# Optimization experiments

Measured on AMD Instinct MI355X. Metric: run time of the kernel, lower is better.

Reference implementation:

```python
import jax, jax.numpy as jnp
import numpy as np

N_SPARSE = 2  # keep N of every M weights (2:4 structured sparsity)
M_SPARSE = 4


def compute_mask(w, n, m):
    # w: [out, in]; zero the (m - n) smallest-|w| entries in each group of m
    out_f, in_f = w.shape
    k = m - n
    wr = jnp.abs(w).reshape(out_f, in_f // m, m)
    # indices of the k smallest |w| per group (torch.topk largest=False)
    _, idx = jax.lax.top_k(-wr, k)                      # [out, in/m, k]
    pruned = jax.nn.one_hot(idx, m, dtype=w.dtype).sum(axis=-2)  # [out, in/m, m]
    mask = 1.0 - pruned
    return mask.reshape(out_f, in_f)


def setup_inputs() -> dict:
    key = jax.random.key(0)
    k1, k2, k3 = jax.random.split(key, 3)
    B, S, Din, Dout = 64, 197, 768, 3072
    x = jax.random.normal(k1, (B, S, Din), dtype=jnp.float32)
    weight = jax.random.normal(k2, (Dout, Din), dtype=jnp.float32)
    bias = jax.random.normal(k3, (Dout,), dtype=jnp.float32)
    return {"x": x, "weight": weight, "bias": bias}


def reference(x, weight, bias):
    # mask is a precomputed buffer in torch (not differentiated)
    mask = compute_mask(jax.lax.stop_gradient(weight), N_SPARSE, M_SPARSE)
    w = weight * mask
    # F.linear: x @ w.T + b
    return jnp.einsum('bsi,oi->bso', x, w) + bias
```

## Files before the change

kernel.cpp:

```cpp
#include <hip/hip_runtime.h>
#include <hip/hip_bf16.h>

#define M_DIM 12608
#define K_DIM 768
#define N_DIM 3072
#define M_PAD 12672
#define BM 128
#define BN 128
#define BK 32

typedef __attribute__((ext_vector_type(8))) short bf16x8;
typedef __attribute__((ext_vector_type(4))) float f32x4;

__device__ __forceinline__ void gload_lds16(const void* g, void* l) {
  __builtin_amdgcn_global_load_lds(
      (const __attribute__((address_space(1))) unsigned int*)g,
      (__attribute__((address_space(3))) unsigned int*)l,
      16, 0, 0);
}

__global__ void cvt_x(const float* __restrict__ x, __hip_bfloat16* __restrict__ xb) {
  size_t i = ((size_t)blockIdx.x * blockDim.x + threadIdx.x) * 8;
  if (i >= (size_t)M_PAD * K_DIM) return;
  union { __hip_bfloat16 h[8]; uint4 u; } o;
  if (i < (size_t)M_DIM * K_DIM) {
    float4 a = *(const float4*)(x + i);
    float4 b = *(const float4*)(x + i + 4);
    o.h[0] = __float2bfloat16(a.x); o.h[1] = __float2bfloat16(a.y);
    o.h[2] = __float2bfloat16(a.z); o.h[3] = __float2bfloat16(a.w);
    o.h[4] = __float2bfloat16(b.x); o.h[5] = __float2bfloat16(b.y);
    o.h[6] = __float2bfloat16(b.z); o.h[7] = __float2bfloat16(b.w);
  } else {
    o.u = make_uint4(0, 0, 0, 0);
  }
  *(uint4*)(xb + i) = o.u;
}

__global__ void cvt_w(const float* __restrict__ w, __hip_bfloat16* __restrict__ wb) {
  size_t g = (size_t)blockIdx.x * blockDim.x + threadIdx.x;
  if (g >= (size_t)N_DIM * (K_DIM / 4)) return;
  float4 v = *(const float4*)(w + g * 4);
  float val[4] = {v.x, v.y, v.z, v.w};
  float a[4] = {fabsf(v.x), fabsf(v.y), fabsf(v.z), fabsf(v.w)};
  union { __hip_bfloat16 h[4]; uint2 u; } o;
#pragma unroll
  for (int i = 0; i < 4; ++i) {
    int rank = 0;
#pragma unroll
    for (int j = 0; j < 4; ++j)
      rank += (a[j] > a[i]) || (a[j] == a[i] && j > i);
    o.h[i] = __float2bfloat16(rank < 2 ? val[i] : 0.0f);
  }
  *(uint2*)(wb + g * 4) = o.u;
}

__global__ __launch_bounds__(256) void gemm_bt(
    const __hip_bfloat16* __restrict__ A,
    const __hip_bfloat16* __restrict__ B,
    const float* __restrict__ bias,
    float* __restrict__ C)
{
  __shared__ char smem[32768];

  const int tid  = threadIdx.x;
  const int lane = tid & 63;
  const int wave = tid >> 6;
  const int wm = wave >> 1, wn = wave & 1;

  const int tile_m = blockIdx.y * BM;
  const int tile_n = blockIdx.x * BN;

  const int ris  = lane >> 2;
  const int slot = lane & 3;
  const int arow0 = wave * 32 + ris;
  const int arow1 = arow0 + 16;
  const int acg0 = slot ^ (arow0 & 3) ^ ((arow0 >> 2) & 3);
  const int acg1 = slot ^ (arow1 & 3) ^ ((arow1 >> 2) & 3);
  const __hip_bfloat16* ag0 = A + (size_t)(tile_m + arow0) * K_DIM + acg0 * 8;
  const __hip_bfloat16* ag1 = A + (size_t)(tile_m + arow1) * K_DIM + acg1 * 8;
  const __hip_bfloat16* bg0 = B + (size_t)(tile_n + arow0) * K_DIM + acg0 * 8;
  const __hip_bfloat16* bg1 = B + (size_t)(tile_n + arow1) * K_DIM + acg1 * 8;

  const int frow  = lane & 15;
  const int fslot = (lane >> 4) ^ (lane & 3) ^ ((lane & 15) >> 2);
  const int aoff = (wm * 64 + frow) * 64 + fslot * 16;
  const int boff = (wn * 64 + frow) * 64 + fslot * 16;

  f32x4 acc[4][4] = {};

  {
    char* ba = smem + wave * 2048;
    char* bb = smem + 8192 + wave * 2048;
    gload_lds16(ag0, ba);
    gload_lds16(ag1, ba + 1024);
    gload_lds16(bg0, bb);
    gload_lds16(bg1, bb + 1024);
  }

  const int NITER = K_DIM / BK;
  for (int k = 0; k < NITER; ++k) {
    const int cur = k & 1;
    __syncthreads();

    if (k + 1 < NITER) {
      const int off = (k + 1) * BK;
      char* ba = smem + (cur ^ 1) * 16384 + wave * 2048;
      char* bb = smem + (cur ^ 1) * 16384 + 8192 + wave * 2048;
      gload_lds16(ag0 + off, ba);
      gload_lds16(ag1 + off, ba + 1024);
      gload_lds16(bg0 + off, bb);
      gload_lds16(bg1 + off, bb + 1024);
    }

    const char* sa = smem + cur * 16384;
    const char* sb = sa + 8192;
    bf16x8 af[4], bfr[4];
#pragma unroll
    for (int i = 0; i < 4; ++i)
      af[i] = *(const bf16x8*)(sa + aoff + i * 1024);
#pragma unroll
    for (int j = 0; j < 4; ++j)
      bfr[j] = *(const bf16x8*)(sb + boff + j * 1024);
#pragma unroll
    for (int i = 0; i < 4; ++i)
#pragma unroll
      for (int j = 0; j < 4; ++j)
        acc[i][j] = __builtin_amdgcn_mfma_f32_16x16x32_bf16(af[i], bfr[j], acc[i][j], 0, 0, 0);
  }

  const int ccol = lane & 15;
  const int quad = lane >> 4;
  float bv[4];
#pragma unroll
  for (int j = 0; j < 4; ++j)
    bv[j] = bias[tile_n + wn * 64 + j * 16 + ccol];

  float* tr = (float*)smem + wave * 1088;
  const int erow = lane >> 2;
  const int eseg = lane & 3;

  #pragma unroll
  for (int i = 0; i < 4; ++i) {
    __syncthreads();
#pragma unroll
    for (int j = 0; j < 4; ++j)
#pragma unroll
      for (int r = 0; r < 4; ++r)
        tr[(quad * 4 + r) * 68 + j * 16 + ccol] = acc[i][j][r] + bv[j];
    __syncthreads();
    const int grow = tile_m + wm * 64 + i * 16 + erow;
    if (grow < M_DIM) {
      float* dst = C + (size_t)grow * N_DIM + tile_n + wn * 64 + eseg * 16;
      const float* src = tr + erow * 68 + eseg * 16;
#pragma unroll
      for (int u = 0; u < 4; ++u)
        *(f32x4*)(dst + u * 4) = *(const f32x4*)(src + u * 4);
    }
  }
}

extern "C" void kernel_launch(void* const* d_in, const int* in_sizes, int n_in,
                              void* d_out, int out_size, void* d_ws, size_t ws_size,
                              hipStream_t stream) {
  const float* x    = (const float*)d_in[0];
  const float* w    = (const float*)d_in[1];
  const float* bias = (const float*)d_in[2];
  float* out = (float*)d_out;

  __hip_bfloat16* xb = (__hip_bfloat16*)d_ws;
  __hip_bfloat16* wb = xb + (size_t)M_PAD * K_DIM;

  cvt_x<<<(M_PAD * K_DIM / 8 + 255) / 256, 256, 0, stream>>>(x, xb);
  cvt_w<<<(N_DIM * (K_DIM / 4) + 255) / 256, 256, 0, stream>>>(w, wb);

  dim3 grid(N_DIM / BN, M_PAD / BM);
  gemm_bt<<<grid, 256, 0, stream>>>(xb, wb, bias, out);
}
```

Measured before the change: 278.6 us.

## Enlarge GEMM tile to 256x128 and fuse the two conversion kernels

The GEMM block tile grows from 128x128 to 256x128. Each of the four waves now owns 64 rows across the full 128 columns, with 4x8 MFMA accumulators, and M is padded to 12800. This raises arithmetic intensity per LDS load and cuts B-tile reloads. The x and weight conversion kernels are merged into one launch to save one kernel launch. The cost is higher register pressure, now hinted with launch_bounds(256,2), more LDS per block, extra padded rows, and fewer blocks in the grid.

```diff
diff --git a/kernel.cpp b/kernel.cpp
--- a/kernel.cpp
+++ b/kernel.cpp
@@ -4,8 +4,8 @@
 #define M_DIM 12608
 #define K_DIM 768
 #define N_DIM 3072
-#define M_PAD 12672
-#define BM 128
+#define M_PAD 12800
+#define BM 256
 #define BN 128
 #define BK 32
 
@@ -19,141 +19,144 @@
       16, 0, 0);
 }
 
-__global__ void cvt_x(const float* __restrict__ x, __hip_bfloat16* __restrict__ xb) {
-  size_t i = ((size_t)blockIdx.x * blockDim.x + threadIdx.x) * 8;
-  if (i >= (size_t)M_PAD * K_DIM) return;
-  union { __hip_bfloat16 h[8]; uint4 u; } o;
-  if (i < (size_t)M_DIM * K_DIM) {
-    float4 a = *(const float4*)(x + i);
-    float4 b = *(const float4*)(x + i + 4);
-    o.h[0] = __float2bfloat16(a.x); o.h[1] = __float2bfloat16(a.y);
-    o.h[2] = __float2bfloat16(a.z); o.h[3] = __float2bfloat16(a.w);
-    o.h[4] = __float2bfloat16(b.x); o.h[5] = __float2bfloat16(b.y);
-    o.h[6] = __float2bfloat16(b.z); o.h[7] = __float2bfloat16(b.w);
+#define GX 4800
+#define GW 2304
+__global__ void cvt_fused(const float* __restrict__ x, const float* __restrict__ w,
+                          __hip_bfloat16* __restrict__ xb, __hip_bfloat16* __restrict__ wb) {
+  if (blockIdx.x < GX) {
+    size_t i = ((size_t)blockIdx.x * 256 + threadIdx.x) * 8;
+    union { __hip_bfloat16 h[8]; uint4 u; } o;
+    if (i < (size_t)M_DIM * K_DIM) {
+      float4 a = *(const float4*)(x + i);
+      float4 b = *(const float4*)(x + i + 4);
+      o.h[0] = __float2bfloat16(a.x); o.h[1] = __float2bfloat16(a.y);
+      o.h[2] = __float2bfloat16(a.z); o.h[3] = __float2bfloat16(a.w);
+      o.h[4] = __float2bfloat16(b.x); o.h[5] = __float2bfloat16(b.y);
+      o.h[6] = __float2bfloat16(b.z); o.h[7] = __float2bfloat16(b.w);
+    } else {
+      o.u = make_uint4(0, 0, 0, 0);
+    }
+    *(uint4*)(xb + i) = o.u;
   } else {
-    o.u = make_uint4(0, 0, 0, 0);
+    size_t g = ((size_t)(blockIdx.x - GX) * 256 + threadIdx.x);
+    float4 v = *(const float4*)(w + g * 4);
+    float val[4] = {v.x, v.y, v.z, v.w};
+    float a[4] = {fabsf(v.x), fabsf(v.y), fabsf(v.z), fabsf(v.w)};
+    union { __hip_bfloat16 h[4]; uint2 u; } o;
+#pragma unroll
+    for (int i = 0; i < 4; ++i) {
+      int rank = 0;
+#pragma unroll
+      for (int j = 0; j < 4; ++j)
+        rank += (a[j] > a[i]) || (a[j] == a[i] && j > i);
+      o.h[i] = __float2bfloat16(rank < 2 ? val[i] : 0.0f);
+    }
+    *(uint2*)(wb + g * 4) = o.u;
   }
-  *(uint4*)(xb + i) = o.u;
 }
 
-__global__ void cvt_w(const float* __restrict__ w, __hip_bfloat16* __restrict__ wb) {
-  size_t g = (size_t)blockIdx.x * blockDim.x + threadIdx.x;
-  if (g >= (size_t)N_DIM * (K_DIM / 4)) return;
-  float4 v = *(const float4*)(w + g * 4);
-  float val[4] = {v.x, v.y, v.z, v.w};
-  float a[4] = {fabsf(v.x), fabsf(v.y), fabsf(v.z), fabsf(v.w)};
-  union { __hip_bfloat16 h[4]; uint2 u; } o;
-#pragma unroll
-  for (int i = 0; i < 4; ++i) {
-    int rank = 0;
-#pragma unroll
-    for (int j = 0; j < 4; ++j)
-      rank += (a[j] > a[i]) || (a[j] == a[i] && j > i);
-    o.h[i] = __float2bfloat16(rank < 2 ? val[i] : 0.0f);
-  }
-  *(uint2*)(wb + g * 4) = o.u;
-}
-
-__global__ __launch_bounds__(256) void gemm_bt(
+__global__ __launch_bounds__(256, 2) void gemm_bt(
     const __hip_bfloat16* __restrict__ A,
     const __hip_bfloat16* __restrict__ B,
     const float* __restrict__ bias,
     float* __restrict__ C)
 {
-  __shared__ char smem[32768];
+  __shared__ char smem[49152];
 
   const int tid  = threadIdx.x;
   const int lane = tid & 63;
   const int wave = tid >> 6;
-  const int wm = wave >> 1, wn = wave & 1;
 
   const int tile_m = blockIdx.y * BM;
   const int tile_n = blockIdx.x * BN;
 
   const int ris  = lane >> 2;
   const int slot = lane & 3;
-  const int arow0 = wave * 32 + ris;
-  const int arow1 = arow0 + 16;
-  const int acg0 = slot ^ (arow0 & 3) ^ ((arow0 >> 2) & 3);
-  const int acg1 = slot ^ (arow1 & 3) ^ ((arow1 >> 2) & 3);
-  const __hip_bfloat16* ag0 = A + (size_t)(tile_m + arow0) * K_DIM + acg0 * 8;
-  const __hip_bfloat16* ag1 = A + (size_t)(tile_m + arow1) * K_DIM + acg1 * 8;
-  const __hip_bfloat16* bg0 = B + (size_t)(tile_n + arow0) * K_DIM + acg0 * 8;
-  const __hip_bfloat16* bg1 = B + (size_t)(tile_n + arow1) * K_DIM + acg1 * 8;
+  const __hip_bfloat16* agp[4];
+  const __hip_bfloat16* bgp[2];
+#pragma unroll
+  for (int i = 0; i < 4; ++i) {
+    const int arow = wave * 64 + i * 16 + ris;
+    const int acg = slot ^ (arow & 3) ^ ((arow >> 2) & 3);
+    agp[i] = A + (size_t)(tile_m + arow) * K_DIM + acg * 8;
+  }
+#pragma unroll
+  for (int i = 0; i < 2; ++i) {
+    const int brow = wave * 32 + i * 16 + ris;
+    const int bcg = slot ^ (brow & 3) ^ ((brow >> 2) & 3);
+    bgp[i] = B + (size_t)(tile_n + brow) * K_DIM + bcg * 8;
+  }
 
   const int frow  = lane & 15;
-  const int fslot = (lane >> 4) ^ (lane & 3) ^ ((lane & 15) >> 2);
-  const int aoff = (wm * 64 + frow) * 64 + fslot * 16;
-  const int boff = (wn * 64 + frow) * 64 + fslot * 16;
+  const int fslot = (lane >> 4) ^ (frow & 3) ^ ((frow >> 2) & 3);
 
-  f32x4 acc[4][4] = {};
+  f32x4 acc[4][8] = {};
 
-  {
-    char* ba = smem + wave * 2048;
-    char* bb = smem + 8192 + wave * 2048;
-    gload_lds16(ag0, ba);
-    gload_lds16(ag1, ba + 1024);
-    gload_lds16(bg0, bb);
-    gload_lds16(bg1, bb + 1024);
-  }
+#pragma unroll
+  for (int i = 0; i < 4; ++i)
+    gload_lds16(agp[i], smem + (wave * 4 + i) * 1024);
+#pragma unroll
+  for (int i = 0; i < 2; ++i)
+    gload_lds16(bgp[i], smem + 16384 + (wave * 2 + i) * 1024);
 
   const int NITER = K_DIM / BK;
+#pragma unroll 2
   for (int k = 0; k < NITER; ++k) {
     const int cur = k & 1;
     __syncthreads();
 
     if (k + 1 < NITER) {
       const int off = (k + 1) * BK;
-      char* ba = smem + (cur ^ 1) * 16384 + wave * 2048;
-      char* bb = smem + (cur ^ 1) * 16384 + 8192 + wave * 2048;
-      gload_lds16(ag0 + off, ba);
-      gload_lds16(ag1 + off, ba + 1024);
-      gload_lds16(bg0 + off, bb);
-      gload_lds16(bg1 + off, bb + 1024);
+      char* bb = smem + (cur ^ 1) * 24576;
+#pragma unroll
+      for (int i = 0; i < 4; ++i)
+        gload_lds16(agp[i] + off, bb + (wave * 4 + i) * 1024);
+#pragma unroll
+      for (int i = 0; i < 2; ++i)
+        gload_lds16(bgp[i] + off, bb + 16384 + (wave * 2 + i) * 1024);
     }
 
-    const char* sa = smem + cur * 16384;
-    const char* sb = sa + 8192;
-    bf16x8 af[4], bfr[4];
+    const char* sa = smem + cur * 24576;
+    bf16x8 af[4], bfr[8];
 #pragma unroll
     for (int i = 0; i < 4; ++i)
-      af[i] = *(const bf16x8*)(sa + aoff + i * 1024);
+      af[i] = *(const bf16x8*)(sa + (wave * 64 + i * 16 + frow) * 64 + fslot * 16);
 #pragma unroll
-    for (int j = 0; j < 4; ++j)
-      bfr[j] = *(const bf16x8*)(sb + boff + j * 1024);
+    for (int j = 0; j < 8; ++j)
+      bfr[j] = *(const bf16x8*)(sa + 16384 + (j * 16 + frow) * 64 + fslot * 16);
 #pragma unroll
     for (int i = 0; i < 4; ++i)
 #pragma unroll
-      for (int j = 0; j < 4; ++j)
+      for (int j = 0; j < 8; ++j)
         acc[i][j] = __builtin_amdgcn_mfma_f32_16x16x32_bf16(af[i], bfr[j], acc[i][j], 0, 0, 0);
   }
 
   const int ccol = lane & 15;
   const int quad = lane >> 4;
-  float bv[4];
+  float bv[8];
 #pragma unroll
-  for (int j = 0; j < 4; ++j)
-    bv[j] = bias[tile_n + wn * 64 + j * 16 + ccol];
+  for (int j = 0; j < 8; ++j)
+    bv[j] = bias[tile_n + j * 16 + ccol];
 
-  float* tr = (float*)smem + wave * 1088;
+  float* tr = (float*)smem + wave * 2112;
   const int erow = lane >> 2;
   const int eseg = lane & 3;
 
-  #pragma unroll
+#pragma unroll
   for (int i = 0; i < 4; ++i) {
     __syncthreads();
 #pragma unroll
-    for (int j = 0; j < 4; ++j)
+    for (int j = 0; j < 8; ++j)
 #pragma unroll
       for (int r = 0; r < 4; ++r)
-        tr[(quad * 4 + r) * 68 + j * 16 + ccol] = acc[i][j][r] + bv[j];
+        tr[(quad * 4 + r) * 132 + j * 16 + ccol] = acc[i][j][r] + bv[j];
     __syncthreads();
-    const int grow = tile_m + wm * 64 + i * 16 + erow;
+    const int grow = tile_m + wave * 64 + i * 16 + erow;
     if (grow < M_DIM) {
-      float* dst = C + (size_t)grow * N_DIM + tile_n + wn * 64 + eseg * 16;
-      const float* src = tr + erow * 68 + eseg * 16;
+      float* dst = C + (size_t)grow * N_DIM + tile_n + eseg * 32;
+      const float* src = tr + erow * 132 + eseg * 32;
 #pragma unroll
-      for (int u = 0; u < 4; ++u)
+      for (int u = 0; u < 8; ++u)
         *(f32x4*)(dst + u * 4) = *(const f32x4*)(src + u * 4);
     }
   }
@@ -170,8 +173,7 @@
   __hip_bfloat16* xb = (__hip_bfloat16*)d_ws;
   __hip_bfloat16* wb = xb + (size_t)M_PAD * K_DIM;
 
-  cvt_x<<<(M_PAD * K_DIM / 8 + 255) / 256, 256, 0, stream>>>(x, xb);
-  cvt_w<<<(N_DIM * (K_DIM / 4) + 255) / 256, 256, 0, stream>>>(w, wb);
+  cvt_fused<<<GX + GW, 256, 0, stream>>>(x, w, xb, wb);
 
   dim3 grid(N_DIM / BN, M_PAD / BM);
   gemm_bt<<<grid, 256, 0, stream>>>(xb, wb, bias, out);
```

Measured after the change: 271.8 us. 2.4% less time.
